# Performance work log

Hardware: AMD Instinct MI355X
Metric: run time of the kernel (lower is better)

## Reference

```python
import jax, jax.numpy as jnp
import numpy as np

B, C, N, O, K = 4, 64, 8192, 128, 20


def setup_inputs() -> dict:
    key = jax.random.key(0)
    k1, k2, k3 = jax.random.split(key, 3)
    x = jax.random.normal(k1, (B, C, N), dtype=jnp.float32)
    # Conv2d(2C, 2C, 1, bias=False) weight squeezed to [2C, 2C]
    W1 = jax.random.normal(k2, (2 * C, 2 * C), dtype=jnp.float32) * (1.0 / np.sqrt(2 * C))
    # Conv2d(2C, O, 1, bias=False) weight squeezed to [O, 2C]
    W2 = jax.random.normal(k3, (O, 2 * C), dtype=jnp.float32) * (1.0 / np.sqrt(2 * C))
    return {"x": x, "W1": W1, "W2": W2, "spiral_size": K}


def _knn_idx(x, k):
    # x: [B, C, N]; negative squared pairwise distance, top-k = k nearest (incl. self)
    inner = -2.0 * jnp.einsum('bcn,bcm->bnm', x, x)          # [B, N, N]
    xx = jnp.sum(x * x, axis=1)                               # [B, N]
    pd = -xx[:, :, None] - inner - xx[:, None, :]             # [B, N, N]
    return jax.lax.top_k(pd, k)[1]                            # [B, N, k] int32


def reference(x, W1, W2, spiral_size):
    b, c, n = x.shape
    idx = _knn_idx(x, spiral_size)                            # [B, N, K]
    xt = jnp.transpose(x, (0, 2, 1))                          # [B, N, C]
    spirals = xt[jnp.arange(b)[:, None, None], idx]           # [B, N, K, C] neighbor gather
    center = jnp.broadcast_to(xt[:, :, None, :], spirals.shape)
    feats = jnp.concatenate([spirals - center, center], axis=-1)  # [B, N, K, 2C]
    h = jnp.einsum('bnkc,dc->bnkd', feats, W1)                # 1x1 conv1
    gate = jax.nn.softmax(h, axis=2)                          # softmax over neighbor dim K
    gated = feats * gate                                      # [B, N, K, 2C]
    out = jnp.einsum('bnkc,oc->bon', gated, W2)               # conv2 + sum over K -> [B, O, N]
    return out
```

## Files before the change

### kernel.cpp

```cpp
#include <hip/hip_runtime.h>
#include <math.h>

#define BB 4
#define CC 64
#define NN 8192
#define OO 128
#define KK 20
#define DD 128
#define BUFSZ 15

typedef short bf16x8 __attribute__((ext_vector_type(8)));
typedef float f32x4 __attribute__((ext_vector_type(4)));
typedef unsigned short u16x8 __attribute__((ext_vector_type(8)));
typedef unsigned long long u64;

typedef __attribute__((address_space(1))) const void gvoid;
typedef __attribute__((address_space(3))) void lvoid;

__device__ __forceinline__ u64 packkey(float v, int idx) {
  unsigned u = __float_as_uint(v);
  unsigned o = ((int)u < 0) ? ~u : (u | 0x80000000u);
  return (((u64)o) << 32) | (unsigned)(~idx);
}
__device__ __forceinline__ float keyval(u64 k) {
  unsigned o = (unsigned)(k >> 32);
  unsigned u = (o & 0x80000000u) ? (o ^ 0x80000000u) : ~o;
  return __uint_as_float(u);
}
#define INITKEY (((u64)0x007FFFFFu) << 32)

__device__ __forceinline__ unsigned short bf_rne(float f) {
  unsigned u = __float_as_uint(f);
  u += 0x7FFFu + ((u >> 16) & 1u);
  return (unsigned short)(u >> 16);
}
__device__ __forceinline__ float bf_f(unsigned short h) {
  return __uint_as_float(((unsigned)h) << 16);
}

__global__ __launch_bounds__(128) void prep_kernel(const float* __restrict__ x,
                                                   float* __restrict__ xx,
                                                   unsigned short* __restrict__ xs) {
  const int tid = threadIdx.x;
  const int b = blockIdx.y;
  const int n0 = blockIdx.x * 128;
  const float* xb = x + (size_t)b * CC * NN;
  float xv[CC];
  float acc = 0.0f;
  #pragma unroll
  for (int c = 0; c < CC; ++c) {
    float v = xb[(size_t)c * NN + n0 + tid];
    acc += v * v;
    xv[c] = v;
  }
  xx[b * NN + n0 + tid] = acc;

  const int n = n0 + tid;
  char* xsrow = ((char*)xs) + ((size_t)b * NN + n) * 384;
  const int swn = (n & 7) << 4;
  #pragma unroll
  for (int gr = 0; gr < 8; ++gr) {
    u16x8 h8, m8, l8;
    #pragma unroll
    for (int e = 0; e < 8; ++e) {
      float v = xv[gr * 8 + e];
      unsigned short h = bf_rne(v);
      float r = v - bf_f(h);
      unsigned short m = bf_rne(r);
      r -= bf_f(m);
      unsigned short l = bf_rne(r);
      h8[e] = (unsigned short)h; m8[e] = m; l8[e] = l;
    }
    *(u16x8*)(xsrow + (((gr * 16) + 0) ^ swn)) = h8;
    *(u16x8*)(xsrow + (((gr * 16) + 128) ^ swn)) = m8;
    *(u16x8*)(xsrow + (((gr * 16) + 256) ^ swn)) = l8;
  }
}

__global__ __launch_bounds__(256, 2) void knn_kernel(
    const unsigned short* __restrict__ xs, const float* __restrict__ xx,
    int* __restrict__ fidx) {
  __shared__ __attribute__((aligned(16))) unsigned short atile[2][64 * 192];
  __shared__ float cxx[2][64];
  __shared__ u64 abuf[4][64][BUFSZ];
  const int tid = threadIdx.x;
  const int w = tid >> 6;
  const int lane = tid & 63;
  const int r = lane & 15;
  const int g = lane >> 4;
  const int b = blockIdx.y;
  const int qbase = blockIdx.x * 64 + w * 16;
  const int q = qbase + r;
  const char* xsb = ((const char*)xs) + (size_t)b * NN * 384;

  bf16x8 bq[3][2];
  {
    const char* qrow = xsb + (size_t)q * 384;
    const int sw = (q & 7) << 4;
    #pragma unroll
    for (int s = 0; s < 3; ++s)
      #pragma unroll
      for (int c = 0; c < 2; ++c)
        bq[s][c] = *(const bf16x8*)(qrow + ((s * 128 + c * 64 + g * 16) ^ sw));
  }
  const float xxq = xx[b * NN + q];

  u64 tk[KK];
  #pragma unroll
  for (int j = 0; j < KK; ++j) tk[j] = INITKEY;
  float minv = -INFINITY;
  int cnt = 0;
  u64* mybuf = &abuf[w][lane][0];

  auto stage = [&](int t, int p) {
    const char* src = xsb + (size_t)t * 64 * 384;
    char* dst = (char*)atile[p];
    #pragma unroll
    for (int it = 0; it < 6; ++it) {
      __builtin_amdgcn_global_load_lds(
          (gvoid*)(src + it * 4096 + tid * 16),
          (lvoid*)(dst + it * 4096 + tid * 16), 16, 0, 0);
    }
    if (tid < 16) {
      __builtin_amdgcn_global_load_lds(
          (gvoid*)(xx + b * NN + t * 64 + tid * 4),
          (lvoid*)(cxx[p] + tid * 4), 16, 0, 0);
    }
  };

  auto rebuild = [&]() {
    int mxc = cnt;
    #pragma unroll
    for (int o = 32; o > 0; o >>= 1) {
      int v = __shfl_xor(mxc, o);
      mxc = mxc > v ? mxc : v;
    }
    for (int i = 0; i < mxc; ++i) {
      u64 k = (i < cnt) ? mybuf[i] : 0ULL;
      if (k > tk[KK - 1]) {
        #pragma unroll
        for (int jj = KK - 1; jj >= 1; --jj)
          tk[jj] = (k > tk[jj - 1]) ? tk[jj - 1] : ((k > tk[jj]) ? k : tk[jj]);
        tk[0] = (k > tk[0]) ? k : tk[0];
      }
    }
    cnt = 0;
    minv = keyval(tk[KK - 1]);
  };

  stage(0, 0);
  __syncthreads();

  for (int t = 0; t < NN / 64; ++t) {
    const int p = t & 1;
    if (t < NN / 64 - 1) stage(t + 1, p ^ 1);

    #pragma unroll
    for (int half = 0; half < 2; ++half) {
      #pragma unroll
      for (int cth = 0; cth < 2; ++cth) {
        const int ct = half * 2 + cth;
        const char* arow = ((const char*)atile[p]) + (ct * 16 + r) * 384;
        const int sw = (r & 7) << 4;
        bf16x8 a6[6];
        #pragma unroll
        for (int c6 = 0; c6 < 6; ++c6)
          a6[c6] = *(const bf16x8*)(arow + ((c6 * 64 + g * 16) ^ sw));
        f32x4 acc = {0.f, 0.f, 0.f, 0.f};
        __builtin_amdgcn_s_setprio(1);
        #pragma unroll
        for (int s = 2; s >= 0; --s)
          #pragma unroll
          for (int c6 = 0; c6 < 6; ++c6)
            acc = __builtin_amdgcn_mfma_f32_16x16x32_bf16(a6[c6], bq[s][c6 & 1],
                                                          acc, 0, 0, 0);
        __builtin_amdgcn_s_setprio(0);
        #pragma unroll
        for (int j = 0; j < 4; ++j) {
          const int ml = ct * 16 + g * 4 + j;
          float pd = (-xxq - (-2.0f * acc[j])) - cxx[p][ml];
          if (pd > minv) { mybuf[cnt] = packkey(pd, t * 64 + ml); ++cnt; }
        }
      }
      if (__any(cnt > 7)) rebuild();
    }
    __syncthreads();
  }

  rebuild();

  u64* ml = ((u64*)&atile[0][0]) + (size_t)w * 64 * KK;
  #pragma unroll
  for (int j = 0; j < KK; ++j) ml[lane * KK + j] = tk[j];
  __syncthreads();
  if (lane < 16) {
    int* fo = fidx + ((size_t)b * NN + qbase + lane) * KK;
    const u64* L0 = ml + (lane + 0) * KK;
    const u64* L1 = ml + (lane + 16) * KK;
    const u64* L2 = ml + (lane + 32) * KK;
    const u64* L3 = ml + (lane + 48) * KK;
    int p0 = 0, p1 = 0, p2 = 0, p3 = 0;
    u64 h0 = L0[0], h1 = L1[0], h2 = L2[0], h3 = L3[0];
    #pragma unroll
    for (int k = 0; k < KK; ++k) {
      u64 bv = h0; int bc = 0;
      if (h1 > bv) { bv = h1; bc = 1; }
      if (h2 > bv) { bv = h2; bc = 2; }
      if (h3 > bv) { bv = h3; bc = 3; }
      fo[k] = (int)(~(unsigned)bv);
      if (bc == 0)      { ++p0; h0 = (p0 < KK) ? L0[p0] : 0ULL; }
      else if (bc == 1) { ++p1; h1 = (p1 < KK) ? L1[p1] : 0ULL; }
      else if (bc == 2) { ++p2; h2 = (p2 < KK) ? L2[p2] : 0ULL; }
      else              { ++p3; h3 = (p3 < KK) ? L3[p3] : 0ULL; }
    }
  }
}

__global__ __launch_bounds__(256) void w1prep_kernel(const float* __restrict__ W1,
                                                     unsigned short* __restrict__ w1p) {
  for (int e = threadIdx.x; e < 12288; e += 256) {
    const int f = e >> 9;
    const int rr = e & 511;
    const int l = rr >> 3;
    const int j = rr & 7;
    const int pair = f / 3, s = f % 3;
    const int dt = pair >> 1, kc = pair & 1;
    const int d = dt * 16 + (l & 15);
    const int c = kc * 32 + (l >> 4) * 8 + j;
    const float v = W1[d * DD + c];
    const unsigned short h = bf_rne(v);
    float r = v - bf_f(h);
    const unsigned short m = bf_rne(r);
    r -= bf_f(m);
    const unsigned short lo = bf_rne(r);
    w1p[(size_t)f * 512 + l * 8 + j] = (s == 0) ? h : ((s == 1) ? m : lo);
  }
}

#define MFMA16(A, B, C) __builtin_amdgcn_mfma_f32_16x16x32_bf16((A), (B), (C), 0, 0, 0)

template <int SA, int SB>
__device__ __forceinline__ void h_term(const bf16x8 (&a)[3][2][2],
                                       const bf16x8 (&w1f)[24],
                                       f32x4 (&acc)[4][2]) {
  #pragma unroll
  for (int dt = 0; dt < 4; ++dt)
    #pragma unroll
    for (int kc = 0; kc < 2; ++kc) {
      const bf16x8 bf = w1f[(dt * 2 + kc) * 3 + SB];
      acc[dt][0] = MFMA16(a[SA][kc][0], bf, acc[dt][0]);
      acc[dt][1] = MFMA16(a[SA][kc][1], bf, acc[dt][1]);
    }
}

template <int DT>
__device__ __forceinline__ float d1_epi(const bf16x8 (&a)[3][2][2],
                                        bf16x8 id0, bf16x8 id1,
                                        const f32x4 (&acc)[4][2], int g) {
  constexpr int KC = DT >> 1;
  const bf16x8 idp = (DT & 1) ? id1 : id0;
  f32x4 yf0 = {0.f, 0.f, 0.f, 0.f}, yf1 = {0.f, 0.f, 0.f, 0.f};
  yf0 = MFMA16(a[1][KC][0], idp, yf0);
  yf0 = MFMA16(a[0][KC][0], idp, yf0);
  yf1 = MFMA16(a[1][KC][1], idp, yf1);
  yf1 = MFMA16(a[0][KC][1], idp, yf1);
  const f32x4 h0 = acc[DT][0], h1 = acc[DT][1];
  float mx = fmaxf(fmaxf(h0[0], h0[1]), fmaxf(h0[2], h0[3]));
  mx = fmaxf(mx, fmaxf(fmaxf(h1[0], h1[1]), fmaxf(h1[2], h1[3])));
  mx = fmaxf(mx, __shfl_xor(mx, 16));
  mx = fmaxf(mx, __shfl_xor(mx, 32));
  float sl = 0.f, tl = 0.f;
  #pragma unroll
  for (int j = 0; j < 4; ++j) {
    const float e = __expf(h0[j] - mx);
    sl += e; tl += yf0[j] * e;
  }
  if (g == 0) {
    #pragma unroll
    for (int j = 0; j < 4; ++j) {
      const float e = __expf(h1[j] - mx);
      sl += e; tl += yf1[j] * e;
    }
  }
  sl += __shfl_xor(sl, 16); sl += __shfl_xor(sl, 32);
  tl += __shfl_xor(tl, 16); tl += __shfl_xor(tl, 32);
  return tl / sl;
}

__global__ __launch_bounds__(256, 2) void d1_kernel(
    const unsigned short* __restrict__ xs, const int* __restrict__ fidx,
    const unsigned short* __restrict__ w1p, float* __restrict__ gbuf) {
  const int tid = threadIdx.x;
  const int w = tid >> 6;
  const int lane = tid & 63;
  const int r = lane & 15;
  const int g = lane >> 4;
  const int b = blockIdx.y;
  const char* xsb = ((const char*)xs) + (size_t)b * NN * 384;

  bf16x8 w1f[24];
  #pragma unroll
  for (int f = 0; f < 24; ++f)
    w1f[f] = *(const bf16x8*)(((const char*)w1p) + f * 1024 + lane * 16);

  bf16x8 id0, id1;
  #pragma unroll
  for (int j = 0; j < 8; ++j) {
    id0[j] = (g == (r >> 3) && j == (r & 7)) ? (short)0x3F80 : (short)0;
    id1[j] = (g == 2 + (r >> 3) && j == (r & 7)) ? (short)0x3F80 : (short)0;
  }

  for (int i = 0; i < 4; ++i) {
    const int n = blockIdx.x * 16 + w * 4 + i;
    const size_t ng = (size_t)b * NN + n;
    const int* kp = fidx + ng * KK;
    const int row0 = kp[r];
    const int row1 = kp[16 + (r & 3)];
    const char* rp0 = xsb + (size_t)row0 * 384;
    const char* rp1 = xsb + (size_t)row1 * 384;
    const int sw0 = (row0 & 7) << 4, sw1 = (row1 & 7) << 4;

    bf16x8 a[3][2][2];
    #pragma unroll
    for (int s = 0; s < 3; ++s)
      #pragma unroll
      for (int kc = 0; kc < 2; ++kc) {
        const int off = s * 128 + kc * 64 + g * 16;
        a[s][kc][0] = *(const bf16x8*)(rp0 + (off ^ sw0));
        a[s][kc][1] = *(const bf16x8*)(rp1 + (off ^ sw1));
      }

    const char* zrow = xsb + (size_t)n * 384;
    const int swn = (n & 7) << 4;
    float zl;
    {
      const unsigned short zh = *(const unsigned short*)(zrow + ((2 * lane) ^ swn));
      const unsigned short zm = *(const unsigned short*)(zrow + ((128 + 2 * lane) ^ swn));
      const unsigned short zo = *(const unsigned short*)(zrow + ((256 + 2 * lane) ^ swn));
      zl = bf_f(zh) + bf_f(zm) + bf_f(zo);
    }

    f32x4 acc[4][2];
    #pragma unroll
    for (int dt = 0; dt < 4; ++dt) {
      acc[dt][0] = (f32x4){0.f, 0.f, 0.f, 0.f};
      acc[dt][1] = (f32x4){0.f, 0.f, 0.f, 0.f};
    }
    h_term<2, 0>(a, w1f, acc);
    h_term<0, 2>(a, w1f, acc);
    h_term<1, 1>(a, w1f, acc);
    h_term<1, 0>(a, w1f, acc);
    h_term<0, 1>(a, w1f, acc);
    h_term<0, 0>(a, w1f, acc);

    const float t0 = d1_epi<0>(a, id0, id1, acc, g);
    const float t1 = d1_epi<1>(a, id0, id1, acc, g);
    const float t2 = d1_epi<2>(a, id0, id1, acc, g);
    const float t3 = d1_epi<3>(a, id0, id1, acc, g);

    float* go = gbuf + ng * DD;
    go[64 + lane] = zl;
    const float z0 = __shfl(zl, r);
    const float z1 = __shfl(zl, 16 + r);
    const float z2 = __shfl(zl, 32 + r);
    const float z3 = __shfl(zl, 48 + r);
    if (lane < 16) {
      go[r]      = t0 - z0;
      go[16 + r] = t1 - z1;
      go[32 + r] = t2 - z2;
      go[48 + r] = t3 - z3;
    }
  }
}

__global__ __launch_bounds__(256) void d2_kernel(const float* __restrict__ gbuf,
                                                 const float* __restrict__ W2,
                                                 float* __restrict__ out) {
  __shared__ float4 w2s[OO * 32];
  const int tid = threadIdx.x;
  const int b = blockIdx.y;
  const int n0 = blockIdx.x * 32;
  const float4* w2v = (const float4*)W2;
  for (int t = tid; t < OO * 32; t += 256) {
    int o = t >> 5, c4 = t & 31;
    w2s[o * 32 + (c4 ^ (o & 7))] = w2v[t];
  }
  __syncthreads();
  const int og = tid & 7;
  const int ni = tid >> 3;
  const int n = n0 + ni;
  const float4* gp = (const float4*)(gbuf + ((size_t)b * NN + n) * DD);
  float acc[16];
  #pragma unroll
  for (int j = 0; j < 16; ++j) acc[j] = 0.0f;
  for (int c4 = 0; c4 < 32; ++c4) {
    float4 g4 = gp[c4];
    #pragma unroll
    for (int j = 0; j < 16; ++j) {
      const int o = j * 8 + og;
      float4 w4 = w2s[o * 32 + (c4 ^ og)];
      acc[j] += g4.x * w4.x + g4.y * w4.y + g4.z * w4.z + g4.w * w4.w;
    }
  }
  float* outb = out + (size_t)b * OO * NN;
  #pragma unroll
  for (int j = 0; j < 16; ++j) {
    outb[(size_t)(j * 8 + og) * NN + n] = acc[j];
  }
}

extern "C" void kernel_launch(void* const* d_in, const int* in_sizes, int n_in,
                              void* d_out, int out_size, void* d_ws, size_t ws_size,
                              hipStream_t stream) {
  const float* x  = (const float*)d_in[0];
  const float* W1 = (const float*)d_in[1];
  const float* W2 = (const float*)d_in[2];
  float* out = (float*)d_out;
  char* ws = (char*)d_ws;
  unsigned short* xs = (unsigned short*)(ws);
  float* xx = (float*)(ws + 12582912);
  unsigned short* w1p = (unsigned short*)(ws + 12582912);
  int* fidx = (int*)(ws + 12713984);
  float* gbuf = (float*)(ws + 15335424);

  prep_kernel<<<dim3(NN / 128, BB), 128, 0, stream>>>(x, xx, xs);
  knn_kernel<<<dim3(NN / 64, BB), 256, 0, stream>>>(xs, xx, fidx);
  w1prep_kernel<<<dim3(1), 256, 0, stream>>>(W1, w1p);
  d1_kernel<<<dim3(NN / 16, BB), 256, 0, stream>>>(xs, fidx, w1p, gbuf);
  d2_kernel<<<dim3(NN / 32, BB), 256, 0, stream>>>(gbuf, W2, out);
}
```

Measured before the change: 791.2 us.

## Split KNN candidate range across two blocks and merge partial top-k

Measured after the change: 708.3 us. 10.5% less time.

```diff
diff --git a/kernel.cpp b/kernel.cpp
--- a/kernel.cpp
+++ b/kernel.cpp
@@ -7,7 +7,8 @@
 #define OO 128
 #define KK 20
 #define DD 128
-#define BUFSZ 15
+#define NT 64
+#define BUFSZ 10
 
 typedef short bf16x8 __attribute__((ext_vector_type(8)));
 typedef float f32x4 __attribute__((ext_vector_type(4)));
@@ -77,20 +78,25 @@
   }
 }
 
-__global__ __launch_bounds__(256, 2) void knn_kernel(
+__global__ __launch_bounds__(256, 4) void knn_kernel(
     const unsigned short* __restrict__ xs, const float* __restrict__ xx,
-    int* __restrict__ fidx) {
-  __shared__ __attribute__((aligned(16))) unsigned short atile[2][64 * 192];
-  __shared__ float cxx[2][64];
-  __shared__ u64 abuf[4][64][BUFSZ];
+    u64* __restrict__ pkeys) {
+  __shared__ __attribute__((aligned(16))) unsigned short atile[64 * 192];
+  __shared__ float pdb[4][64][BUFSZ];
+  __shared__ unsigned short idb[4][64][BUFSZ];
+  __shared__ float cxx[64];
   const int tid = threadIdx.x;
   const int w = tid >> 6;
   const int lane = tid & 63;
   const int r = lane & 15;
   const int g = lane >> 4;
-  const int b = blockIdx.y;
-  const int qbase = blockIdx.x * 64 + w * 16;
+  const int lin = blockIdx.x;
+  const int b = (lin & 7) >> 1;
+  const int ch = lin & 1;
+  const int qg = lin >> 3;
+  const int qbase = qg * 64 + w * 16;
   const int q = qbase + r;
+  const int cbase = ch * 4096;
   const char* xsb = ((const char*)xs) + (size_t)b * NN * 384;
 
   bf16x8 bq[3][2];
@@ -110,11 +116,12 @@
   for (int j = 0; j < KK; ++j) tk[j] = INITKEY;
   float minv = -INFINITY;
   int cnt = 0;
-  u64* mybuf = &abuf[w][lane][0];
-
-  auto stage = [&](int t, int p) {
-    const char* src = xsb + (size_t)t * 64 * 384;
-    char* dst = (char*)atile[p];
+  float* pdl = &pdb[w][lane][0];
+  unsigned short* idl = &idb[w][lane][0];
+
+  auto stage = [&](int t) {
+    const char* src = xsb + (size_t)(cbase + t * 64) * 384;
+    char* dst = (char*)atile;
     #pragma unroll
     for (int it = 0; it < 6; ++it) {
       __builtin_amdgcn_global_load_lds(
@@ -123,8 +130,8 @@
     }
     if (tid < 16) {
       __builtin_amdgcn_global_load_lds(
-          (gvoid*)(xx + b * NN + t * 64 + tid * 4),
-          (lvoid*)(cxx[p] + tid * 4), 16, 0, 0);
+          (gvoid*)(xx + b * NN + cbase + t * 64 + tid * 4),
+          (lvoid*)(cxx + tid * 4), 16, 0, 0);
     }
   };
 
@@ -136,7 +143,7 @@
       mxc = mxc > v ? mxc : v;
     }
     for (int i = 0; i < mxc; ++i) {
-      u64 k = (i < cnt) ? mybuf[i] : 0ULL;
+      u64 k = (i < cnt) ? packkey(pdl[i], (int)idl[i]) : 0ULL;
       if (k > tk[KK - 1]) {
         #pragma unroll
         for (int jj = KK - 1; jj >= 1; --jj)
@@ -148,71 +155,89 @@
     minv = keyval(tk[KK - 1]);
   };
 
-  stage(0, 0);
-  __syncthreads();
-
-  for (int t = 0; t < NN / 64; ++t) {
-    const int p = t & 1;
-    if (t < NN / 64 - 1) stage(t + 1, p ^ 1);
-
-    #pragma unroll
-    for (int half = 0; half < 2; ++half) {
-      #pragma unroll
-      for (int cth = 0; cth < 2; ++cth) {
-        const int ct = half * 2 + cth;
-        const char* arow = ((const char*)atile[p]) + (ct * 16 + r) * 384;
-        const int sw = (r & 7) << 4;
-        bf16x8 a6[6];
+  for (int t = 0; t < NT; ++t) {
+    stage(t);
+    __syncthreads();
+
+    #pragma unroll
+    for (int ct = 0; ct < 4; ++ct) {
+      const char* arow = ((const char*)atile) + (ct * 16 + r) * 384;
+      const int sw = (r & 7) << 4;
+      bf16x8 a6[6];
+      #pragma unroll
+      for (int c6 = 0; c6 < 6; ++c6)
+        a6[c6] = *(const bf16x8*)(arow + ((c6 * 64 + g * 16) ^ sw));
+      f32x4 acc = {0.f, 0.f, 0.f, 0.f};
+      __builtin_amdgcn_s_setprio(1);
+      #pragma unroll
+      for (int s = 2; s >= 0; --s)
         #pragma unroll
         for (int c6 = 0; c6 < 6; ++c6)
-          a6[c6] = *(const bf16x8*)(arow + ((c6 * 64 + g * 16) ^ sw));
-        f32x4 acc = {0.f, 0.f, 0.f, 0.f};
-        __builtin_amdgcn_s_setprio(1);
-        #pragma unroll
-        for (int s = 2; s >= 0; --s)
-          #pragma unroll
-          for (int c6 = 0; c6 < 6; ++c6)
-            acc = __builtin_amdgcn_mfma_f32_16x16x32_bf16(a6[c6], bq[s][c6 & 1],
-                                                          acc, 0, 0, 0);
-        __builtin_amdgcn_s_setprio(0);
-        #pragma unroll
-        for (int j = 0; j < 4; ++j) {
-          const int ml = ct * 16 + g * 4 + j;
-          float pd = (-xxq - (-2.0f * acc[j])) - cxx[p][ml];
-          if (pd > minv) { mybuf[cnt] = packkey(pd, t * 64 + ml); ++cnt; }
+          acc = __builtin_amdgcn_mfma_f32_16x16x32_bf16(a6[c6], bq[s][c6 & 1],
+                                                        acc, 0, 0, 0);
+      __builtin_amdgcn_s_setprio(0);
+      #pragma unroll
+      for (int j = 0; j < 4; ++j) {
+        const int ml = ct * 16 + g * 4 + j;
+        float pd = (-xxq - (-2.0f * acc[j])) - cxx[ml];
+        if (pd > minv) {
+          pdl[cnt] = pd;
+          idl[cnt] = (unsigned short)(cbase + t * 64 + ml);
+          ++cnt;
         }
       }
-      if (__any(cnt > 7)) rebuild();
+      if (__any(cnt > 6)) rebuild();
     }
     __syncthreads();
   }
 
   rebuild();
 
-  u64* ml = ((u64*)&atile[0][0]) + (size_t)w * 64 * KK;
-  #pragma unroll
-  for (int j = 0; j < KK; ++j) ml[lane * KK + j] = tk[j];
-  __syncthreads();
-  if (lane < 16) {
-    int* fo = fidx + ((size_t)b * NN + qbase + lane) * KK;
-    const u64* L0 = ml + (lane + 0) * KK;
-    const u64* L1 = ml + (lane + 16) * KK;
-    const u64* L2 = ml + (lane + 32) * KK;
-    const u64* L3 = ml + (lane + 48) * KK;
-    int p0 = 0, p1 = 0, p2 = 0, p3 = 0;
-    u64 h0 = L0[0], h1 = L1[0], h2 = L2[0], h3 = L3[0];
-    #pragma unroll
-    for (int k = 0; k < KK; ++k) {
-      u64 bv = h0; int bc = 0;
-      if (h1 > bv) { bv = h1; bc = 1; }
-      if (h2 > bv) { bv = h2; bc = 2; }
-      if (h3 > bv) { bv = h3; bc = 3; }
-      fo[k] = (int)(~(unsigned)bv);
-      if (bc == 0)      { ++p0; h0 = (p0 < KK) ? L0[p0] : 0ULL; }
-      else if (bc == 1) { ++p1; h1 = (p1 < KK) ? L1[p1] : 0ULL; }
-      else if (bc == 2) { ++p2; h2 = (p2 < KK) ? L2[p2] : 0ULL; }
-      else              { ++p3; h3 = (p3 < KK) ? L3[p3] : 0ULL; }
-    }
+  for (int pass = 0; pass < 2; ++pass) {
+    if (pass) __syncthreads();
+    if ((w >> 1) == pass) {
+      u64* ml = ((u64*)atile) + (size_t)(w & 1) * 64 * KK;
+      #pragma unroll
+      for (int j = 0; j < KK; ++j) ml[lane * KK + j] = tk[j];
+      if (lane < 16) {
+        u64* po = pkeys + (((size_t)b * NN + qbase + lane) * 2 + ch) * KK;
+        const u64* L0 = ml + (lane + 0) * KK;
+        const u64* L1 = ml + (lane + 16) * KK;
+        const u64* L2 = ml + (lane + 32) * KK;
+        const u64* L3 = ml + (lane + 48) * KK;
+        int p0 = 0, p1 = 0, p2 = 0, p3 = 0;
+        u64 h0 = L0[0], h1 = L1[0], h2 = L2[0], h3 = L3[0];
+        #pragma unroll
+        for (int k = 0; k < KK; ++k) {
+          u64 bv = h0; int bc = 0;
+          if (h1 > bv) { bv = h1; bc = 1; }
+          if (h2 > bv) { bv = h2; bc = 2; }
+          if (h3 > bv) { bv = h3; bc = 3; }
+          po[k] = bv;
+          if (bc == 0)      { ++p0; h0 = (p0 < KK) ? L0[p0] : 0ULL; }
+          else if (bc == 1) { ++p1; h1 = (p1 < KK) ? L1[p1] : 0ULL; }
+          else if (bc == 2) { ++p2; h2 = (p2 < KK) ? L2[p2] : 0ULL; }
+          else              { ++p3; h3 = (p3 < KK) ? L3[p3] : 0ULL; }
+        }
+      }
+    }
+  }
+}
+
+__global__ __launch_bounds__(256) void merge_kernel(const u64* __restrict__ pkeys,
+                                                    int* __restrict__ fidx) {
+  const int q = blockIdx.x * 256 + threadIdx.x;
+  const u64* pk = pkeys + (size_t)q * 2 * KK;
+  int* fo = fidx + (size_t)q * KK;
+  int p0 = 0, p1 = 0;
+  u64 h0 = pk[0], h1 = pk[KK];
+  #pragma unroll
+  for (int k = 0; k < KK; ++k) {
+    const bool t1 = h1 > h0;
+    const u64 bv = t1 ? h1 : h0;
+    fo[k] = (int)(~(unsigned)bv);
+    if (t1) { ++p1; h1 = (p1 < KK) ? pk[KK + p1] : 0ULL; }
+    else    { ++p0; h0 = (p0 < KK) ? pk[p0] : 0ULL; }
   }
 }
 
@@ -421,10 +446,12 @@
   float* xx = (float*)(ws + 12582912);
   unsigned short* w1p = (unsigned short*)(ws + 12582912);
   int* fidx = (int*)(ws + 12713984);
+  u64* pkeys = (u64*)(ws + 15335424);
   float* gbuf = (float*)(ws + 15335424);
 
   prep_kernel<<<dim3(NN / 128, BB), 128, 0, stream>>>(x, xx, xs);
-  knn_kernel<<<dim3(NN / 64, BB), 256, 0, stream>>>(xs, xx, fidx);
+  knn_kernel<<<dim3(1024), 256, 0, stream>>>(xs, xx, pkeys);
+  merge_kernel<<<dim3(BB * NN / 256), 256, 0, stream>>>(pkeys, fidx);
   w1prep_kernel<<<dim3(1), 256, 0, stream>>>(W1, w1p);
   d1_kernel<<<dim3(NN / 16, BB), 256, 0, stream>>>(xs, fidx, w1p, gbuf);
   d2_kernel<<<dim3(NN / 32, BB), 256, 0, stream>>>(gbuf, W2, out);
```

## Split KNN candidate range into four chunks with a separate merge kernel

Applied to the files above, without the earlier changes.

Result: slower. 2.898 ms (+266.3%).

```diff
diff --git a/kernel.cpp b/kernel.cpp
--- a/kernel.cpp
+++ b/kernel.cpp
@@ -7,7 +7,12 @@
 #define OO 128
 #define KK 20
 #define DD 128
-#define BUFSZ 15
+#define NCH 4
+#define CH (NN / NCH)
+#define TC 32
+#define NT (CH / TC)
+#define QB 128
+#define BUFSZ 8
 
 typedef short bf16x8 __attribute__((ext_vector_type(8)));
 typedef float f32x4 __attribute__((ext_vector_type(4)));
@@ -77,20 +82,28 @@
   }
 }
 
-__global__ __launch_bounds__(256, 2) void knn_kernel(
+__global__ __launch_bounds__(512, 8) void knn_kernel(
     const unsigned short* __restrict__ xs, const float* __restrict__ xx,
-    int* __restrict__ fidx) {
-  __shared__ __attribute__((aligned(16))) unsigned short atile[2][64 * 192];
-  __shared__ float cxx[2][64];
-  __shared__ u64 abuf[4][64][BUFSZ];
+    float* __restrict__ pval, unsigned short* __restrict__ pidx) {
+  __shared__ __attribute__((aligned(16))) unsigned short atile[TC * 192];
+  __shared__ __attribute__((aligned(16))) char bufmem[8 * 64 * BUFSZ * 6];
+  __shared__ float cxx[TC];
+  float* pdb = (float*)bufmem;
+  unsigned short* idb = (unsigned short*)(bufmem + 8 * 64 * BUFSZ * 4);
+
   const int tid = threadIdx.x;
   const int w = tid >> 6;
   const int lane = tid & 63;
   const int r = lane & 15;
   const int g = lane >> 4;
-  const int b = blockIdx.y;
-  const int qbase = blockIdx.x * 64 + w * 16;
+  const int lin = blockIdx.x;
+  const int xcd = lin & 7;
+  const int b = xcd >> 1;
+  const int ch = ((xcd & 1) << 1) | ((lin >> 3) & 1);
+  const int qg = lin >> 4;
+  const int qbase = qg * QB + w * 16;
   const int q = qbase + r;
+  const int cbase = ch * CH;
   const char* xsb = ((const char*)xs) + (size_t)b * NN * 384;
 
   bf16x8 bq[3][2];
@@ -110,22 +123,20 @@
   for (int j = 0; j < KK; ++j) tk[j] = INITKEY;
   float minv = -INFINITY;
   int cnt = 0;
-  u64* mybuf = &abuf[w][lane][0];
-
-  auto stage = [&](int t, int p) {
-    const char* src = xsb + (size_t)t * 64 * 384;
-    char* dst = (char*)atile[p];
-    #pragma unroll
-    for (int it = 0; it < 6; ++it) {
-      __builtin_amdgcn_global_load_lds(
-          (gvoid*)(src + it * 4096 + tid * 16),
-          (lvoid*)(dst + it * 4096 + tid * 16), 16, 0, 0);
-    }
-    if (tid < 16) {
-      __builtin_amdgcn_global_load_lds(
-          (gvoid*)(xx + b * NN + t * 64 + tid * 4),
-          (lvoid*)(cxx[p] + tid * 4), 16, 0, 0);
-    }
+  float* pdl = pdb + (w * 64 + lane) * BUFSZ;
+  unsigned short* idl = idb + (w * 64 + lane) * BUFSZ;
+
+  auto stage = [&](int t) {
+    const char* src = xsb + (size_t)(cbase + t * TC) * 384;
+    char* dst = (char*)atile;
+    __builtin_amdgcn_global_load_lds((gvoid*)(src + tid * 16),
+                                     (lvoid*)(dst + tid * 16), 16, 0, 0);
+    if (tid < 256)
+      __builtin_amdgcn_global_load_lds((gvoid*)(src + 8192 + tid * 16),
+                                       (lvoid*)(dst + 8192 + tid * 16), 16, 0, 0);
+    if (tid < 8)
+      __builtin_amdgcn_global_load_lds((gvoid*)(xx + b * NN + cbase + t * TC + tid * 4),
+                                       (lvoid*)(cxx + tid * 4), 16, 0, 0);
   };
 
   auto rebuild = [&]() {
@@ -136,7 +147,7 @@
       mxc = mxc > v ? mxc : v;
     }
     for (int i = 0; i < mxc; ++i) {
-      u64 k = (i < cnt) ? mybuf[i] : 0ULL;
+      u64 k = (i < cnt) ? packkey(pdl[i], (int)idl[i]) : 0ULL;
       if (k > tk[KK - 1]) {
         #pragma unroll
         for (int jj = KK - 1; jj >= 1; --jj)
@@ -148,71 +159,102 @@
     minv = keyval(tk[KK - 1]);
   };
 
-  stage(0, 0);
-  __syncthreads();
-
-  for (int t = 0; t < NN / 64; ++t) {
-    const int p = t & 1;
-    if (t < NN / 64 - 1) stage(t + 1, p ^ 1);
-
-    #pragma unroll
-    for (int half = 0; half < 2; ++half) {
+  for (int t = 0; t < NT; ++t) {
+    stage(t);
+    __syncthreads();
+
+    #pragma unroll
+    for (int ct = 0; ct < 2; ++ct) {
+      const char* arow = ((const char*)atile) + (ct * 16 + r) * 384;
+      const int sw = (r & 7) << 4;
+      bf16x8 a6[6];
       #pragma unroll
-      for (int cth = 0; cth < 2; ++cth) {
-        const int ct = half * 2 + cth;
-        const char* arow = ((const char*)atile[p]) + (ct * 16 + r) * 384;
-        const int sw = (r & 7) << 4;
-        bf16x8 a6[6];
+      for (int c6 = 0; c6 < 6; ++c6)
+        a6[c6] = *(const bf16x8*)(arow + ((c6 * 64 + g * 16) ^ sw));
+      f32x4 acc = {0.f, 0.f, 0.f, 0.f};
+      __builtin_amdgcn_s_setprio(1);
+      #pragma unroll
+      for (int s = 2; s >= 0; --s)
         #pragma unroll
         for (int c6 = 0; c6 < 6; ++c6)
-          a6[c6] = *(const bf16x8*)(arow + ((c6 * 64 + g * 16) ^ sw));
-        f32x4 acc = {0.f, 0.f, 0.f, 0.f};
-        __builtin_amdgcn_s_setprio(1);
+          acc = __builtin_amdgcn_mfma_f32_16x16x32_bf16(a6[c6], bq[s][c6 & 1],
+                                                        acc, 0, 0, 0);
+      __builtin_amdgcn_s_setprio(0);
+
+      float pd0 = (-xxq - (-2.0f * acc[0])) - cxx[ct * 16 + g * 4 + 0];
+      float pd1 = (-xxq - (-2.0f * acc[1])) - cxx[ct * 16 + g * 4 + 1];
+      float pd2 = (-xxq - (-2.0f * acc[2])) - cxx[ct * 16 + g * 4 + 2];
+      float pd3 = (-xxq - (-2.0f * acc[3])) - cxx[ct * 16 + g * 4 + 3];
+      const float maxpd = fmaxf(fmaxf(pd0, pd1), fmaxf(pd2, pd3));
+      if (__any(maxpd > minv)) {
+        const int i0 = cbase + t * TC + ct * 16 + g * 4;
+        if (pd0 > minv) { pdl[cnt] = pd0; idl[cnt] = (unsigned short)(i0 + 0); ++cnt; }
+        if (pd1 > minv) { pdl[cnt] = pd1; idl[cnt] = (unsigned short)(i0 + 1); ++cnt; }
+        if (pd2 > minv) { pdl[cnt] = pd2; idl[cnt] = (unsigned short)(i0 + 2); ++cnt; }
+        if (pd3 > minv) { pdl[cnt] = pd3; idl[cnt] = (unsigned short)(i0 + 3); ++cnt; }
+        if (__any(cnt > BUFSZ - 4)) rebuild();
+      }
+    }
+    __syncthreads();
+  }
+
+  rebuild();
+
+  for (int pass = 0; pass < 4; ++pass) {
+    __syncthreads();
+    if ((w >> 1) == pass) {
+      u64* ml = ((u64*)bufmem) + (size_t)(w & 1) * 64 * KK;
+      #pragma unroll
+      for (int j = 0; j < KK; ++j) ml[lane * KK + j] = tk[j];
+      if (lane < 16) {
+        const size_t qn = (size_t)b * NN + qbase + lane;
+        float* po = pval + (qn * NCH + ch) * KK;
+        unsigned short* io = pidx + (qn * NCH + ch) * KK;
+        const u64* L0 = ml + (lane + 0) * KK;
+        const u64* L1 = ml + (lane + 16) * KK;
+        const u64* L2 = ml + (lane + 32) * KK;
+        const u64* L3 = ml + (lane + 48) * KK;
+        int p0 = 0, p1 = 0, p2 = 0, p3 = 0;
+        u64 h0 = L0[0], h1 = L1[0], h2 = L2[0], h3 = L3[0];
         #pragma unroll
-        for (int s = 2; s >= 0; --s)
-          #pragma unroll
-          for (int c6 = 0; c6 < 6; ++c6)
-            acc = __builtin_amdgcn_mfma_f32_16x16x32_bf16(a6[c6], bq[s][c6 & 1],
-                                                          acc, 0, 0, 0);
-        __builtin_amdgcn_s_setprio(0);
-        #pragma unroll
-        for (int j = 0; j < 4; ++j) {
-          const int ml = ct * 16 + g * 4 + j;
-          float pd = (-xxq - (-2.0f * acc[j])) - cxx[p][ml];
-          if (pd > minv) { mybuf[cnt] = packkey(pd, t * 64 + ml); ++cnt; }
+        for (int k = 0; k < KK; ++k) {
+          u64 bv = h0; int bc = 0;
+          if (h1 > bv) { bv = h1; bc = 1; }
+          if (h2 > bv) { bv = h2; bc = 2; }
+          if (h3 > bv) { bv = h3; bc = 3; }
+          po[k] = keyval(bv);
+          io[k] = (unsigned short)(~(unsigned)bv);
+          if (bc == 0)      { ++p0; h0 = (p0 < KK) ? L0[p0] : 0ULL; }
+          else if (bc == 1) { ++p1; h1 = (p1 < KK) ? L1[p1] : 0ULL; }
+          else if (bc == 2) { ++p2; h2 = (p2 < KK) ? L2[p2] : 0ULL; }
+          else              { ++p3; h3 = (p3 < KK) ? L3[p3] : 0ULL; }
         }
       }
-      if (__any(cnt > 7)) rebuild();
-    }
-    __syncthreads();
-  }
-
-  rebuild();
-
-  u64* ml = ((u64*)&atile[0][0]) + (size_t)w * 64 * KK;
-  #pragma unroll
-  for (int j = 0; j < KK; ++j) ml[lane * KK + j] = tk[j];
-  __syncthreads();
-  if (lane < 16) {
-    int* fo = fidx + ((size_t)b * NN + qbase + lane) * KK;
-    const u64* L0 = ml + (lane + 0) * KK;
-    const u64* L1 = ml + (lane + 16) * KK;
-    const u64* L2 = ml + (lane + 32) * KK;
-    const u64* L3 = ml + (lane + 48) * KK;
-    int p0 = 0, p1 = 0, p2 = 0, p3 = 0;
-    u64 h0 = L0[0], h1 = L1[0], h2 = L2[0], h3 = L3[0];
-    #pragma unroll
-    for (int k = 0; k < KK; ++k) {
-      u64 bv = h0; int bc = 0;
-      if (h1 > bv) { bv = h1; bc = 1; }
-      if (h2 > bv) { bv = h2; bc = 2; }
-      if (h3 > bv) { bv = h3; bc = 3; }
-      fo[k] = (int)(~(unsigned)bv);
-      if (bc == 0)      { ++p0; h0 = (p0 < KK) ? L0[p0] : 0ULL; }
-      else if (bc == 1) { ++p1; h1 = (p1 < KK) ? L1[p1] : 0ULL; }
-      else if (bc == 2) { ++p2; h2 = (p2 < KK) ? L2[p2] : 0ULL; }
-      else              { ++p3; h3 = (p3 < KK) ? L3[p3] : 0ULL; }
-    }
+    }
+  }
+}
+
+__global__ __launch_bounds__(256) void merge_kernel(const float* __restrict__ pval,
+                                                    const unsigned short* __restrict__ pidx,
+                                                    int* __restrict__ fidx) {
+  const int qn = blockIdx.x * 256 + threadIdx.x;
+  const float* pv = pval + (size_t)qn * NCH * KK;
+  const unsigned short* pi = pidx + (size_t)qn * NCH * KK;
+  int* fo = fidx + (size_t)qn * KK;
+  int p0 = 0, p1 = 0, p2 = 0, p3 = 0;
+  float v0 = pv[0], v1 = pv[KK], v2 = pv[2 * KK], v3 = pv[3 * KK];
+  int i0 = pi[0], i1 = pi[KK], i2 = pi[2 * KK], i3 = pi[3 * KK];
+  #pragma unroll
+  for (int k = 0; k < KK; ++k) {
+    float bv = v0; int bi = i0; int bc = 0;
+    if (v1 > bv || (v1 == bv && i1 < bi)) { bv = v1; bi = i1; bc = 1; }
+    if (v2 > bv || (v2 == bv && i2 < bi)) { bv = v2; bi = i2; bc = 2; }
+    if (v3 > bv || (v3 == bv && i3 < bi)) { bv = v3; bi = i3; bc = 3; }
+    fo[k] = bi;
+    if (bc == 0)      { ++p0; v0 = (p0 < KK) ? pv[p0] : -INFINITY;          i0 = (p0 < KK) ? pi[p0] : 0x7fffffff; }
+    else if (bc == 1) { ++p1; v1 = (p1 < KK) ? pv[KK + p1] : -INFINITY;     i1 = (p1 < KK) ? pi[KK + p1] : 0x7fffffff; }
+    else if (bc == 2) { ++p2; v2 = (p2 < KK) ? pv[2 * KK + p2] : -INFINITY; i2 = (p2 < KK) ? pi[2 * KK + p2] : 0x7fffffff; }
+    else              { ++p3; v3 = (p3 < KK) ? pv[3 * KK + p3] : -INFINITY; i3 = (p3 < KK) ? pi[3 * KK + p3] : 0x7fffffff; }
   }
 }
 
@@ -421,10 +463,13 @@
   float* xx = (float*)(ws + 12582912);
   unsigned short* w1p = (unsigned short*)(ws + 12582912);
   int* fidx = (int*)(ws + 12713984);
+  float* pval = (float*)(ws + 15335424);
+  unsigned short* pidx = (unsigned short*)(ws + 25821184);
   float* gbuf = (float*)(ws + 15335424);
 
   prep_kernel<<<dim3(NN / 128, BB), 128, 0, stream>>>(x, xx, xs);
-  knn_kernel<<<dim3(NN / 64, BB), 256, 0, stream>>>(xs, xx, fidx);
+  knn_kernel<<<dim3(1024), 512, 0, stream>>>(xs, xx, pval, pidx);
+  merge_kernel<<<dim3(BB * NN / 256), 256, 0, stream>>>(pval, pidx, fidx);
   w1prep_kernel<<<dim3(1), 256, 0, stream>>>(W1, w1p);
   d1_kernel<<<dim3(NN / 16, BB), 256, 0, stream>>>(xs, fidx, w1p, gbuf);
   d2_kernel<<<dim3(NN / 32, BB), 256, 0, stream>>>(gbuf, W2, out);
```
